# Kernel tuning notes

Measured on AMD Instinct MI355X. Metric: run time of the kernel, lower is better.

The kernel has to match this reference:

```python
import jax, jax.numpy as jnp
import numpy as np

N_NODES = 10000
N_EDGES = 640000
D_IN = 128
D_INTER = 128


def gcn_conv(x, edge_index, edge_weight, W, b):
    # PyG GCNConv: out = D^{-1/2} (A + I) D^{-1/2} (X W) + b
    n = x.shape[0]
    h = x @ W  # [N, D_out]
    row, col = edge_index[0], edge_index[1]  # source, target
    loop = jnp.arange(n, dtype=row.dtype)
    row = jnp.concatenate([row, loop])
    col = jnp.concatenate([col, loop])
    ew = jnp.concatenate([edge_weight, jnp.ones((n,), edge_weight.dtype)])
    deg = jax.ops.segment_sum(ew, col, num_segments=n)  # in-degree incl. self loops
    dinv = jnp.where(deg > 0, jax.lax.rsqrt(deg), jnp.zeros_like(deg))
    norm = dinv[row] * ew * dinv[col]  # [E+N]
    msgs = norm[:, None] * h[row]  # gather + scale
    out = jax.ops.segment_sum(msgs, col, num_segments=n)  # scatter-add aggregate
    return out + b


def setup_inputs() -> dict:
    key = jax.random.key(0)
    ks = jax.random.split(key, 8)
    x = jax.random.normal(ks[0], (N_NODES, D_IN), dtype=jnp.float32)
    edge_index = jax.random.randint(ks[1], (2, N_EDGES), 0, N_NODES, dtype=jnp.int64)
    edge_weight = jax.random.uniform(ks[2], (N_EDGES,), dtype=jnp.float32)
    # Glorot-ish init for linear weights, zeros for bias (PyG default)
    s1 = 1.0 / np.sqrt(D_IN)
    s2 = 1.0 / np.sqrt(D_INTER)
    W1 = jax.random.uniform(ks[3], (D_IN, D_INTER), jnp.float32, -s1, s1)
    b1 = jnp.zeros((D_INTER,), jnp.float32)
    W2 = jax.random.uniform(ks[4], (D_INTER, D_IN), jnp.float32, -s2, s2)
    b2 = jnp.zeros((D_IN,), jnp.float32)
    return {"x": x, "edge_index": edge_index, "edge_weight": edge_weight,
            "W1": W1, "b1": b1, "W2": W2, "b2": b2}


def reference(x, edge_index, edge_weight, W1, b1, W2, b2):
    # GCN.forward in eval mode: dropout is identity
    h = jax.nn.relu(gcn_conv(x, edge_index, edge_weight, W1, b1))
    out = jax.nn.relu(gcn_conv(h, edge_index, edge_weight, W2, b2))
    return out
```

## Files before the change

### kernel.cpp

```cpp
#include <hip/hip_runtime.h>

#define NN 10000
#define NE 640000
#define D  128
#define PAD_SHIFT 7
#define GEMM_BLOCKS ((NN + 31) / 32)
#define CSTRIDE 10240

__device__ __forceinline__ int xcc_id() {
    unsigned x;
    asm volatile("s_getreg_b32 %0, hwreg(HW_REG_XCC_ID)" : "=s"(x));
    return (int)(x & 7);
}


__global__ __launch_bounds__(256) void zero_kernel(int* __restrict__ p, int n) {
    int i = blockIdx.x * 256 + threadIdx.x;
    if (i < n) p[i] = 0;
}


__global__ __launch_bounds__(256) void fused_gemm_count_kernel(const float* __restrict__ X,
                                                               const float* __restrict__ W,
                                                               float* __restrict__ H,
                                                               const int* __restrict__ ei,
                                                               int* __restrict__ cnt8,
                                                               int* __restrict__ rank) {
    int bid = blockIdx.x;
    if (bid < GEMM_BLOCKS) {
        __shared__ float xs[32][D];
        int t  = threadIdx.x;
        int d  = t & 127;
        int rh = t >> 7;
        int r0 = bid * 32;
#pragma unroll
        for (int r = 0; r < 16; ++r) {
            int rr = r0 + rh * 16 + r;
            xs[rh * 16 + r][d] = (rr < NN) ? X[(size_t)rr * D + d] : 0.0f;
        }
        __syncthreads();
        float acc[16];
#pragma unroll
        for (int r = 0; r < 16; ++r) acc[r] = 0.0f;
        for (int k = 0; k < D; k += 4) {
            float w0 = W[(k + 0) * D + d];
            float w1 = W[(k + 1) * D + d];
            float w2 = W[(k + 2) * D + d];
            float w3 = W[(k + 3) * D + d];
#pragma unroll
            for (int r = 0; r < 16; ++r) {
                float4 xv = *reinterpret_cast<const float4*>(&xs[rh * 16 + r][k]);
                acc[r] = fmaf(xv.x, w0, acc[r]);
                acc[r] = fmaf(xv.y, w1, acc[r]);
                acc[r] = fmaf(xv.z, w2, acc[r]);
                acc[r] = fmaf(xv.w, w3, acc[r]);
            }
        }
#pragma unroll
        for (int r = 0; r < 16; ++r) {
            int rr = r0 + rh * 16 + r;
            if (rr < NN) H[(size_t)rr * D + d] = acc[r];
        }
    } else {
        int e = (bid - GEMM_BLOCKS) * 256 + threadIdx.x;
        if (e < NE) {
            int c = ei[NE + e];
            int x = xcc_id();
            int lr = __hip_atomic_fetch_add(&cnt8[x * CSTRIDE + c], 1,
                                            __ATOMIC_RELAXED,
                                            __HIP_MEMORY_SCOPE_WORKGROUP);
            rank[e] = (x << 16) | lr;
        }
    }
}


__global__ __launch_bounds__(256) void base_kernel(int* __restrict__ cnt8,
                                                   int* __restrict__ cnt) {
    int n = blockIdx.x * 256 + threadIdx.x;
    if (n >= NN) return;
    int b = 0;
#pragma unroll
    for (int x = 0; x < 8; ++x) {
        int t = cnt8[x * CSTRIDE + n];
        cnt8[x * CSTRIDE + n] = b;
        b += t;
    }
    cnt[n] = b;
}


__global__ __launch_bounds__(256) void scatter_kernel(const int* __restrict__ ei,
                                                      const float* __restrict__ ew,
                                                      const int* __restrict__ rank,
                                                      const int* __restrict__ base8,
                                                      int2* __restrict__ epack) {
    int e = blockIdx.x * 256 + threadIdx.x;
    if (e < NE) {
        int c  = ei[NE + e];
        int rk = rank[e];
        int x  = rk >> 16;
        int lr = rk & 0xFFFF;
        int2 v;
        v.x = ei[e];
        v.y = __float_as_int(ew[e]);
        epack[((size_t)c << PAD_SHIFT) + base8[x * CSTRIDE + c] + lr] = v;
    }
}


__global__ __launch_bounds__(256) void degdinv_kernel(const int* __restrict__ cnt,
                                                      const int2* __restrict__ epack,
                                                      float* __restrict__ dinv) {
    int node = blockIdx.x * 4 + (threadIdx.x >> 6);
    if (node >= NN) return;
    int lane = threadIdx.x & 63;
    int m = cnt[node];
    const int2* base = epack + ((size_t)node << PAD_SHIFT);
    float s = 0.0f;
    for (int j = lane; j < m; j += 64) s += __int_as_float(base[j].y);
#pragma unroll
    for (int off = 32; off; off >>= 1) s += __shfl_down(s, off);
    if (lane == 0) dinv[node] = rsqrtf(s + 1.0f);
}


__global__ __launch_bounds__(256) void gemm_kernel(const float* __restrict__ X,
                                                   const float* __restrict__ W,
                                                   float* __restrict__ H) {
    __shared__ float xs[32][D];
    int t  = threadIdx.x;
    int d  = t & 127;
    int rh = t >> 7;
    int r0 = blockIdx.x * 32;
#pragma unroll
    for (int r = 0; r < 16; ++r) {
        int rr = r0 + rh * 16 + r;
        xs[rh * 16 + r][d] = (rr < NN) ? X[(size_t)rr * D + d] : 0.0f;
    }
    __syncthreads();
    float acc[16];
#pragma unroll
    for (int r = 0; r < 16; ++r) acc[r] = 0.0f;
    for (int k = 0; k < D; k += 4) {
        float w0 = W[(k + 0) * D + d];
        float w1 = W[(k + 1) * D + d];
        float w2 = W[(k + 2) * D + d];
        float w3 = W[(k + 3) * D + d];
#pragma unroll
        for (int r = 0; r < 16; ++r) {
            float4 xv = *reinterpret_cast<const float4*>(&xs[rh * 16 + r][k]);
            acc[r] = fmaf(xv.x, w0, acc[r]);
            acc[r] = fmaf(xv.y, w1, acc[r]);
            acc[r] = fmaf(xv.z, w2, acc[r]);
            acc[r] = fmaf(xv.w, w3, acc[r]);
        }
    }
#pragma unroll
    for (int r = 0; r < 16; ++r) {
        int rr = r0 + rh * 16 + r;
        if (rr < NN) H[(size_t)rr * D + d] = acc[r];
    }
}


__global__ __launch_bounds__(256) void agg_kernel(const float* __restrict__ H,
                                                  const int* __restrict__ cnt,
                                                  const int2* __restrict__ epack,
                                                  const float* __restrict__ dinv,
                                                  const float* __restrict__ bias,
                                                  float* __restrict__ out) {
    int node = blockIdx.x * 8 + (threadIdx.x >> 5);
    if (node >= NN) return;
    int q = threadIdx.x & 31;
    int m = cnt[node];
    const int2* eb = epack + ((size_t)node << PAD_SHIFT);
    const float4* Hq = reinterpret_cast<const float4*>(H) + q;
    float di = dinv[node];

    float4 hc = Hq[(size_t)node * 32];
    float4 acc;
    acc.x = di * hc.x; acc.y = di * hc.y; acc.z = di * hc.z; acc.w = di * hc.w;

    int j = 0;
    for (; j + 8 <= m; j += 8) {
        int   s[8];
        float n[8];
#pragma unroll
        for (int k = 0; k < 8; ++k) {
            int2 v = eb[j + k];
            s[k] = v.x;
            n[k] = dinv[v.x] * __int_as_float(v.y);
        }
#pragma unroll
        for (int k = 0; k < 8; ++k) {
            float4 hv = Hq[(size_t)s[k] * 32];
            acc.x = fmaf(n[k], hv.x, acc.x);
            acc.y = fmaf(n[k], hv.y, acc.y);
            acc.z = fmaf(n[k], hv.z, acc.z);
            acc.w = fmaf(n[k], hv.w, acc.w);
        }
    }
    for (; j < m; ++j) {
        int2 v = eb[j];
        float nn = dinv[v.x] * __int_as_float(v.y);
        float4 hv = Hq[(size_t)v.x * 32];
        acc.x = fmaf(nn, hv.x, acc.x);
        acc.y = fmaf(nn, hv.y, acc.y);
        acc.z = fmaf(nn, hv.z, acc.z);
        acc.w = fmaf(nn, hv.w, acc.w);
    }

    float4 b4 = reinterpret_cast<const float4*>(bias)[q];
    float4 o;
    o.x = fmaxf(fmaf(di, acc.x, b4.x), 0.f);
    o.y = fmaxf(fmaf(di, acc.y, b4.y), 0.f);
    o.z = fmaxf(fmaf(di, acc.z, b4.z), 0.f);
    o.w = fmaxf(fmaf(di, acc.w, b4.w), 0.f);
    reinterpret_cast<float4*>(out)[(size_t)node * 32 + q] = o;
}


extern "C" void kernel_launch(void* const* d_in, const int* in_sizes, int n_in,
                              void* d_out, int out_size, void* d_ws, size_t ws_size,
                              hipStream_t stream) {
    const float* x  = (const float*)d_in[0];
    const int*   ei = (const int*)  d_in[1];
    const float* ew = (const float*)d_in[2];
    const float* W1 = (const float*)d_in[3];
    const float* b1 = (const float*)d_in[4];
    const float* W2 = (const float*)d_in[5];
    const float* b2 = (const float*)d_in[6];
    float* out = (float*)d_out;

    char* ws = (char*)d_ws;
    size_t off = 0;
    auto alloc = [&](size_t bytes) {
        void* p = ws + off;
        off = (off + bytes + 255) & ~(size_t)255;
        return p;
    };
    int*   cnt8  = (int*)  alloc(8 * CSTRIDE * 4);
    int*   cnt   = (int*)  alloc(NN * 4);
    float* dinv  = (float*)alloc(NN * 4);
    int*   rank  = (int*)  alloc((size_t)NE * 4);
    int2*  epack = (int2*) alloc(((size_t)NN << PAD_SHIFT) * 8);
    float* h     = (float*)alloc((size_t)NN * D * 4);
    float* g     = (float*)alloc((size_t)NN * D * 4);

    zero_kernel<<<(8 * CSTRIDE + 255) / 256, 256, 0, stream>>>(cnt8, 8 * CSTRIDE);
    fused_gemm_count_kernel<<<GEMM_BLOCKS + (NE + 255) / 256, 256, 0, stream>>>(
        x, W1, h, ei, cnt8, rank);
    base_kernel   <<<(NN + 255) / 256, 256, 0, stream>>>(cnt8, cnt);
    scatter_kernel<<<(NE + 255) / 256, 256, 0, stream>>>(ei, ew, rank, cnt8, epack);
    degdinv_kernel<<<(NN + 3) / 4, 256, 0, stream>>>(cnt, epack, dinv);

    agg_kernel <<<(NN + 7) / 8, 256, 0, stream>>>(h, cnt, epack, dinv, b1, g);
    gemm_kernel<<<(NN + 31) / 32, 256, 0, stream>>>(g, W2, h);
    agg_kernel <<<(NN + 7) / 8, 256, 0, stream>>>(h, cnt, epack, dinv, b2, out);
}
```

Before: 146.3 us.

## Use per-node feature-parallel aggregation kernel for first layer

Adds a new aggregation kernel that assigns one 128-thread block per node, one thread per feature. It stages the node's edge list and normalization factors in shared memory and then does scalar gathers of neighbor rows. The new kernel handles the first layer, while the second layer keeps the original float4 warp-per-node kernel. The counting atomic also changes from an explicit workgroup-scope relaxed atomic to a plain atomicAdd. That may widen its scope and cost, and could affect correctness on multi-XCC parts. The new kernel assumes node degree fits within 128 padded slots and loses float4 vectorisation on the gathers.

New measurement: 141.7 us. 1.03x faster.

```diff
diff --git a/kernel.cpp b/kernel.cpp
--- a/kernel.cpp
+++ b/kernel.cpp
@@ -66,9 +66,7 @@
         if (e < NE) {
             int c = ei[NE + e];
             int x = xcc_id();
-            int lr = __hip_atomic_fetch_add(&cnt8[x * CSTRIDE + c], 1,
-                                            __ATOMIC_RELAXED,
-                                            __HIP_MEMORY_SCOPE_WORKGROUP);
+            int lr = atomicAdd(&cnt8[x * CSTRIDE + c], 1);
             rank[e] = (x << 16) | lr;
         }
     }
@@ -164,12 +162,44 @@
 }
 
 
-__global__ __launch_bounds__(256) void agg_kernel(const float* __restrict__ H,
-                                                  const int* __restrict__ cnt,
-                                                  const int2* __restrict__ epack,
-                                                  const float* __restrict__ dinv,
-                                                  const float* __restrict__ bias,
-                                                  float* __restrict__ out) {
+__global__ __launch_bounds__(128) void agg_feat_kernel(const float* __restrict__ H,
+                                                       const int* __restrict__ cnt,
+                                                       const int2* __restrict__ epack,
+                                                       const float* __restrict__ dinv,
+                                                       const float* __restrict__ bias,
+                                                       float* __restrict__ out) {
+    __shared__ int   s_src[128];
+    __shared__ float s_n[128];
+    int c = blockIdx.x;
+    int d = threadIdx.x;
+    int m = cnt[c];
+    const int2* eb = epack + ((size_t)c << PAD_SHIFT);
+    float di = dinv[c];
+    if (d < m) {
+        int2 v = eb[d];
+        s_src[d] = v.x;
+        s_n[d]   = dinv[v.x] * __int_as_float(v.y);
+    }
+    __syncthreads();
+    float acc = di * H[(size_t)c * D + d];
+    int jj = 0;
+    for (; jj + 8 <= m; jj += 8) {
+#pragma unroll
+        for (int k = 0; k < 8; ++k)
+            acc = fmaf(s_n[jj + k], H[(size_t)s_src[jj + k] * D + d], acc);
+    }
+    for (; jj < m; ++jj)
+        acc = fmaf(s_n[jj], H[(size_t)s_src[jj] * D + d], acc);
+    out[(size_t)c * D + d] = fmaxf(fmaf(di, acc, bias[d]), 0.0f);
+}
+
+
+__global__ __launch_bounds__(256) void agg_vec_kernel(const float* __restrict__ H,
+                                                      const int* __restrict__ cnt,
+                                                      const int2* __restrict__ epack,
+                                                      const float* __restrict__ dinv,
+                                                      const float* __restrict__ bias,
+                                                      float* __restrict__ out) {
     int node = blockIdx.x * 8 + (threadIdx.x >> 5);
     if (node >= NN) return;
     int q = threadIdx.x & 31;
@@ -255,7 +285,7 @@
     scatter_kernel<<<(NE + 255) / 256, 256, 0, stream>>>(ei, ew, rank, cnt8, epack);
     degdinv_kernel<<<(NN + 3) / 4, 256, 0, stream>>>(cnt, epack, dinv);
 
-    agg_kernel <<<(NN + 7) / 8, 256, 0, stream>>>(h, cnt, epack, dinv, b1, g);
-    gemm_kernel<<<(NN + 31) / 32, 256, 0, stream>>>(g, W2, h);
-    agg_kernel <<<(NN + 7) / 8, 256, 0, stream>>>(h, cnt, epack, dinv, b2, out);
-}
+    agg_feat_kernel<<<NN, 128, 0, stream>>>(h, cnt, epack, dinv, b1, g);
+    gemm_kernel    <<<(NN + 31) / 32, 256, 0, stream>>>(g, W2, h);
+    agg_vec_kernel <<<(NN + 7) / 8, 256, 0, stream>>>(h, cnt, epack, dinv, b2, out);
+}
```
